# Optimization experiments

Hardware: AMD Instinct MI355X
Metric: run time of the kernel (lower is better)

The kernel has to match this reference:

```python
import jax, jax.numpy as jnp
import numpy as np

D = 1024      # model_dim
H = 16        # n_heads
BLOCK = 256   # block_dim
B, S = 4, 4096


def setup_inputs() -> dict:
    key = jax.random.key(0)
    ks = jax.random.split(key, 6)
    x = jax.random.normal(ks[0], (B, S, D), dtype=jnp.float32)
    # random permutation per batch row (mirrors torch.argsort(torch.rand(...)))
    rand_perm = jnp.argsort(jax.random.uniform(ks[1], (B, S)), axis=-1).astype(jnp.int32)
    W_in = jax.random.normal(ks[2], (D, 3 * D), dtype=jnp.float32) / np.float32(np.sqrt(D))
    b_in = jax.random.normal(ks[3], (3 * D,), dtype=jnp.float32) * 0.02
    W_out = jax.random.normal(ks[4], (D, D), dtype=jnp.float32) / np.float32(np.sqrt(D))
    b_out = jax.random.normal(ks[5], (D,), dtype=jnp.float32) * 0.02
    return {"x": x, "rand_perm": rand_perm, "W_in": W_in, "b_in": b_in,
            "W_out": W_out, "b_out": b_out}


def reference(x, rand_perm, W_in, b_in, W_out, b_out):
    Bb, Ss, Dm = x.shape
    dh = Dm // H
    nb = Ss // BLOCK  # S divisible by BLOCK -> no padding needed
    # permute sequence: x_rand[..., i, :] = x[..., perm[i], :]
    x_r = jnp.take_along_axis(x, rand_perm[..., None], axis=-2)          # [B,S,D]
    xb = x_r.reshape(Bb, nb, BLOCK, Dm)                                   # block-diagonal chunks
    qkv = jnp.einsum('bntd,de->bnte', xb, W_in) + b_in                    # [B,nb,blk,3D]
    # torch layout: chunk by head first, then (q,k,v) within head
    qkv = qkv.reshape(Bb, nb, BLOCK, H, 3, dh)
    q = jnp.moveaxis(qkv[..., 0, :], 3, 2)                                # [B,nb,H,blk,dh]
    k = jnp.moveaxis(qkv[..., 1, :], 3, 2)
    v = jnp.moveaxis(qkv[..., 2, :], 3, 2)
    scores = jnp.einsum('bnhtd,bnhsd->bnhts', q, k) / np.float32(np.sqrt(dh))
    att = jax.nn.softmax(scores, axis=-1)
    o = jnp.einsum('bnhts,bnhsd->bnhtd', att, v)                          # [B,nb,H,blk,dh]

    def merge(t):  # [B,nb,H,blk,dh] -> [B,S,D] (heads concatenated on feature dim)
        return jnp.moveaxis(t, 2, 3).reshape(Bb, Ss, Dm)

    o = merge(o) @ W_out + b_out
    k_f = merge(k)
    v_f = merge(v)
    # scatter back: out[perm[i]] = src[i]  <=>  out[j] = src[inv_perm[j]]
    inv = jnp.argsort(rand_perm, axis=-1)
    unperm = lambda t: jnp.take_along_axis(t, inv[..., None], axis=-2)
    return unperm(o), unperm(k_f), unperm(v_f)
```

## Files before the change

### kernel.cpp

```cpp
#include <hip/hip_runtime.h>

#define D_   1024
#define H_   16
#define DHd  64
#define BLK  256
#define B_   4
#define S_   4096
#define NB_  16
#define M_   16384
#define N1_  3072
#define NT_  32

typedef __attribute__((ext_vector_type(8))) short short8;
typedef __attribute__((ext_vector_type(4))) float f32x4;
typedef unsigned short u16;
typedef __attribute__((ext_vector_type(4))) unsigned short u16x4;

__device__ inline u16 f2bf(float f) {
  unsigned int u = __float_as_uint(f);
  unsigned int r = (u + 0x7fffu + ((u >> 16) & 1u)) >> 16;
  return (u16)r;
}

__device__ inline void async_ld16(const void* g, void* l) {
  __builtin_amdgcn_global_load_lds(
      (const __attribute__((address_space(1))) unsigned int*)g,
      (__attribute__((address_space(3))) unsigned int*)l, 16, 0, 0);
}

__global__ __launch_bounds__(256)
void permute_cast_kernel(const float* __restrict__ x, const int* __restrict__ perm,
                         u16* __restrict__ xp) {
  int bid = blockIdx.x;
  int b = bid >> 12;
  int i = bid & 4095;
  int prow = perm[b * S_ + i];
  const float4* src = reinterpret_cast<const float4*>(x + (size_t)(b * S_ + prow) * D_);
  float4 v = src[threadIdx.x];
  u16x4 o;
  o.x = f2bf(v.x); o.y = f2bf(v.y); o.z = f2bf(v.z); o.w = f2bf(v.w);
  reinterpret_cast<u16x4*>(xp + (size_t)bid * D_)[threadIdx.x] = o;
}

__global__ __launch_bounds__(256)
void transpose_cast_kernel(const float* __restrict__ src, u16* __restrict__ dst,
                           int R, int C) {
  __shared__ float tile[32][33];
  int tx = threadIdx.x, ty = threadIdx.y;
  int c0 = blockIdx.x * 32, r0 = blockIdx.y * 32;
  #pragma unroll
  for (int i = ty; i < 32; i += 8)
    tile[i][tx] = src[(size_t)(r0 + i) * C + c0 + tx];
  __syncthreads();
  #pragma unroll
  for (int i = ty; i < 32; i += 8)
    dst[(size_t)(c0 + i) * R + r0 + tx] = f2bf(tile[tx][i]);
}

template<int MODE>
__global__ __launch_bounds__(512, 2)
void gemm_kernel(const u16* __restrict__ A, const u16* __restrict__ BT,
                 const float* __restrict__ bias, const int* __restrict__ perm,
                 u16* __restrict__ q_ws, u16* __restrict__ k_ws, u16* __restrict__ vT_ws,
                 float* __restrict__ out_k, float* __restrict__ out_v,
                 float* __restrict__ out_o) {
  constexpr int NCOL = (MODE == 0) ? N1_ : D_;
  constexpr int NWG  = (M_ / 256) * (NCOL / 256);
  constexpr int CPX  = NWG / 8;

  __shared__ u16 LDS[4 * 16384];
  __shared__ int perm_l[256];

  const int tid  = threadIdx.x;
  const int lane = tid & 63;
  const int w    = tid >> 6;
  const int wr   = w >> 2, wc = w & 3;
  const int l4   = lane >> 4, l15 = lane & 15;

  const int orig = blockIdx.x;
  const int lid  = (orig & 7) * CPX + (orig >> 3);
  const int i0   = (lid & 63) * 256;
  const int n0   = (lid >> 6) * 256;
  const int bidx = i0 >> 12;

  if (tid < 256) perm_l[tid] = perm[bidx * S_ + (i0 & 4095) + tid];

  const int srow = tid >> 2;
  const int sq   = (tid & 3) ^ ((tid >> 3) & 3);
  const u16* pA0 = A  + (size_t)(i0 + srow) * 1024 + sq * 8;
  const u16* pA1 = pA0 + (size_t)128 * 1024;
  const u16* pB0 = BT + (size_t)(n0 + srow) * 1024 + sq * 8;
  const u16* pB1 = pB0 + (size_t)128 * 1024;

  const int ps   = l4 ^ ((l15 >> 1) & 3);
  const int aoff = (wr * 128 + l15) * 64 + ps * 16;
  const int boff = 16384 + (wc * 64 + l15) * 64 + ps * 16;

  f32x4 acc[8][4] = {};

  #define STAGE(kt, b) do {                                    \
    const int ko_ = (kt) * 32;                                 \
    u16* base_ = &LDS[(b) * 16384 + w * 512];                  \
    async_ld16(pA0 + ko_, base_);                              \
    async_ld16(pA1 + ko_, base_ + 4096);                       \
    async_ld16(pB0 + ko_, base_ + 8192);                       \
    async_ld16(pB1 + ko_, base_ + 12288);                      \
  } while (0)

  #define COMPUTE(b) do {                                                         \
    const char* lb_ = (const char*)LDS + (b) * 32768;                             \
    short8 af_[8], bf_[4];                                                        \
    _Pragma("unroll")                                                             \
    for (int m = 0; m < 8; ++m)                                                   \
      af_[m] = *reinterpret_cast<const short8*>(lb_ + aoff + m * 1024);           \
    bf_[0] = *reinterpret_cast<const short8*>(lb_ + boff);                        \
    bf_[1] = *reinterpret_cast<const short8*>(lb_ + boff + 1024);                 \
    __builtin_amdgcn_s_setprio(1);                                                \
    _Pragma("unroll")                                                             \
    for (int m = 0; m < 8; ++m) {                                                 \
      acc[m][0] = __builtin_amdgcn_mfma_f32_16x16x32_bf16(af_[m], bf_[0], acc[m][0], 0, 0, 0); \
      acc[m][1] = __builtin_amdgcn_mfma_f32_16x16x32_bf16(af_[m], bf_[1], acc[m][1], 0, 0, 0); \
    }                                                                             \
    __builtin_amdgcn_s_setprio(0);                                                \
    bf_[2] = *reinterpret_cast<const short8*>(lb_ + boff + 2048);                 \
    bf_[3] = *reinterpret_cast<const short8*>(lb_ + boff + 3072);                 \
    __builtin_amdgcn_s_setprio(1);                                                \
    _Pragma("unroll")                                                             \
    for (int m = 0; m < 8; ++m) {                                                 \
      acc[m][2] = __builtin_amdgcn_mfma_f32_16x16x32_bf16(af_[m], bf_[2], acc[m][2], 0, 0, 0); \
      acc[m][3] = __builtin_amdgcn_mfma_f32_16x16x32_bf16(af_[m], bf_[3], acc[m][3], 0, 0, 0); \
    }                                                                             \
    __builtin_amdgcn_s_setprio(0);                                                \
  } while (0)

  STAGE(0, 0);
  STAGE(1, 1);
  #pragma unroll 1
  for (int kt = 0; kt < NT_ - 2; ++kt) {
    STAGE(kt + 2, (kt + 2) & 3);
    asm volatile("s_waitcnt vmcnt(8) lgkmcnt(0)" ::: "memory");
    __builtin_amdgcn_s_barrier();
    COMPUTE(kt & 3);
  }
  asm volatile("s_waitcnt vmcnt(4) lgkmcnt(0)" ::: "memory");
  __builtin_amdgcn_s_barrier();
  COMPUTE((NT_ - 2) & 3);
  asm volatile("s_waitcnt vmcnt(0) lgkmcnt(0)" ::: "memory");
  __builtin_amdgcn_s_barrier();
  COMPUTE((NT_ - 1) & 3);
  #undef STAGE
  #undef COMPUTE

  if (MODE == 0) {
    #pragma unroll
    for (int n = 0; n < 4; ++n) {
      int col = n0 + wc * 64 + n * 16 + l15;
      float bias_v = bias[col];
      int h  = col / 192;
      int rem = col - h * 192;
      int cc = rem >> 6;
      int dd = rem & 63;
      int qcol = (h << 6) + dd;
      #pragma unroll
      for (int m = 0; m < 8; ++m) {
        int rbase = i0 + wr * 128 + m * 16 + l4 * 4;
        if (cc == 0) {
          #pragma unroll
          for (int r = 0; r < 4; ++r) {
            float val = acc[m][n][r] + bias_v;
            q_ws[(size_t)(rbase + r) * D_ + qcol] = f2bf(val);
          }
        } else if (cc == 1) {
          #pragma unroll
          for (int r = 0; r < 4; ++r) {
            float val = acc[m][n][r] + bias_v;
            int rr = rbase + r;
            k_ws[(size_t)rr * D_ + qcol] = f2bf(val);
            int prow = perm_l[rr - i0];
            out_k[(size_t)(bidx * S_ + prow) * D_ + qcol] = val;
          }
        } else {
          u16x4 pk;
          #pragma unroll
          for (int r = 0; r < 4; ++r) {
            float val = acc[m][n][r] + bias_v;
            int rr = rbase + r;
            int prow = perm_l[rr - i0];
            out_v[(size_t)(bidx * S_ + prow) * D_ + qcol] = val;
            pk[r] = f2bf(val);
          }
          int i_loc = rbase & 4095;
          int nblk = i_loc >> 8;
          int t    = i_loc & 255;
          *reinterpret_cast<u16x4*>(
              &vT_ws[((((size_t)bidx * NB_ + nblk) * H_ + h) * DHd + dd) * BLK + t]) = pk;
        }
      }
    }
  } else {
    #pragma unroll
    for (int n = 0; n < 4; ++n) {
      int col = n0 + wc * 64 + n * 16 + l15;
      float bias_v = bias[col];
      #pragma unroll
      for (int m = 0; m < 8; ++m) {
        int rbase = i0 + wr * 128 + m * 16 + l4 * 4;
        #pragma unroll
        for (int r = 0; r < 4; ++r) {
          int rr = rbase + r;
          int prow = perm_l[rr - i0];
          out_o[(size_t)(bidx * S_ + prow) * D_ + col] = acc[m][n][r] + bias_v;
        }
      }
    }
  }
}

__global__ __launch_bounds__(256)
void attn_kernel(const u16* __restrict__ q_ws, const u16* __restrict__ k_ws,
                 const u16* __restrict__ vT_ws, u16* __restrict__ o_ws) {
  __shared__ u16 P_lds[4 * 64 * 64];

  int bid  = blockIdx.x;
  int h    = bid & 15;
  int nblk = (bid >> 4) & 15;
  int b    = bid >> 8;
  int row0 = b * S_ + nblk * BLK;
  int lane = threadIdx.x & 63;
  int w    = threadIdx.x >> 6;
  int l4 = lane >> 4, l15 = lane & 15;

  const u16* qb  = q_ws + (size_t)row0 * D_ + h * 64;
  const u16* kb  = k_ws + (size_t)row0 * D_ + h * 64;
  const u16* vTb = vT_ws + ((size_t)(b * NB_ + nblk) * H_ + h) * (size_t)(DHd * BLK);

  short8 qf[4][2];
  #pragma unroll
  for (int mt = 0; mt < 4; ++mt)
    #pragma unroll
    for (int kk = 0; kk < 2; ++kk)
      qf[mt][kk] = *reinterpret_cast<const short8*>(
          qb + (size_t)(w * 64 + mt * 16 + l15) * D_ + kk * 32 + l4 * 8);

  f32x4 Oacc[4][4] = {};
  float mS[4][4], lS[4][4];
  #pragma unroll
  for (int mt = 0; mt < 4; ++mt)
    #pragma unroll
    for (int r = 0; r < 4; ++r) { mS[mt][r] = -1e30f; lS[mt][r] = 0.f; }

  for (int ct = 0; ct < 4; ++ct) {
    f32x4 Sc[4][4] = {};
    #pragma unroll
    for (int kk = 0; kk < 2; ++kk) {
      #pragma unroll
      for (int nt = 0; nt < 4; ++nt) {
        short8 kf = *reinterpret_cast<const short8*>(
            kb + (size_t)(ct * 64 + nt * 16 + l15) * D_ + kk * 32 + l4 * 8);
        #pragma unroll
        for (int mt = 0; mt < 4; ++mt)
          Sc[mt][nt] = __builtin_amdgcn_mfma_f32_16x16x32_bf16(qf[mt][kk], kf, Sc[mt][nt], 0, 0, 0);
      }
    }
    #pragma unroll
    for (int mt = 0; mt < 4; ++mt) {
      #pragma unroll
      for (int r = 0; r < 4; ++r) {
        float v0 = fmaxf(fmaxf(Sc[mt][0][r], Sc[mt][1][r]), fmaxf(Sc[mt][2][r], Sc[mt][3][r]));
        v0 *= 0.125f;
        v0 = fmaxf(v0, __shfl_xor(v0, 1));
        v0 = fmaxf(v0, __shfl_xor(v0, 2));
        v0 = fmaxf(v0, __shfl_xor(v0, 4));
        v0 = fmaxf(v0, __shfl_xor(v0, 8));
        float mn = fmaxf(mS[mt][r], v0);
        float alpha = __expf(mS[mt][r] - mn);
        mS[mt][r] = mn;
        float rs = 0.f;
        #pragma unroll
        for (int nt = 0; nt < 4; ++nt) {
          float p = __expf(Sc[mt][nt][r] * 0.125f - mn);
          Sc[mt][nt][r] = p;
          rs += p;
        }
        rs += __shfl_xor(rs, 1);
        rs += __shfl_xor(rs, 2);
        rs += __shfl_xor(rs, 4);
        rs += __shfl_xor(rs, 8);
        lS[mt][r] = lS[mt][r] * alpha + rs;
        #pragma unroll
        for (int nt = 0; nt < 4; ++nt)
          Oacc[mt][nt][r] *= alpha;
      }
    }
    #pragma unroll
    for (int mt = 0; mt < 4; ++mt)
      #pragma unroll
      for (int nt = 0; nt < 4; ++nt)
        #pragma unroll
        for (int r = 0; r < 4; ++r)
          P_lds[w * 4096 + (mt * 16 + l4 * 4 + r) * 64 + nt * 16 + l15] = f2bf(Sc[mt][nt][r]);
    #pragma unroll
    for (int kk = 0; kk < 2; ++kk) {
      short8 pa[4];
      #pragma unroll
      for (int mt = 0; mt < 4; ++mt)
        pa[mt] = *reinterpret_cast<const short8*>(
            &P_lds[w * 4096 + (mt * 16 + l15) * 64 + kk * 32 + l4 * 8]);
      #pragma unroll
      for (int nt = 0; nt < 4; ++nt) {
        short8 vf = *reinterpret_cast<const short8*>(
            vTb + (size_t)(nt * 16 + l15) * BLK + ct * 64 + kk * 32 + l4 * 8);
        #pragma unroll
        for (int mt = 0; mt < 4; ++mt)
          Oacc[mt][nt] = __builtin_amdgcn_mfma_f32_16x16x32_bf16(pa[mt], vf, Oacc[mt][nt], 0, 0, 0);
      }
    }
  }
  u16* ob = o_ws + (size_t)row0 * D_ + h * 64;
  #pragma unroll
  for (int mt = 0; mt < 4; ++mt)
    #pragma unroll
    for (int r = 0; r < 4; ++r) {
      float inv = 1.f / lS[mt][r];
      int row = w * 64 + mt * 16 + l4 * 4 + r;
      #pragma unroll
      for (int nt = 0; nt < 4; ++nt)
        ob[(size_t)row * D_ + nt * 16 + l15] = f2bf(Oacc[mt][nt][r] * inv);
    }
}

extern "C" void kernel_launch(void* const* d_in, const int* in_sizes, int n_in,
                              void* d_out, int out_size, void* d_ws, size_t ws_size,
                              hipStream_t stream) {
  const float* x     = (const float*)d_in[0];
  const int*   perm  = (const int*)d_in[1];
  const float* W_in  = (const float*)d_in[2];
  const float* b_in  = (const float*)d_in[3];
  const float* W_out = (const float*)d_in[4];
  const float* b_out = (const float*)d_in[5];

  float* out_o = (float*)d_out;
  float* out_k = out_o + (size_t)M_ * D_;
  float* out_v = out_k + (size_t)M_ * D_;

  const size_t nE = (size_t)M_ * D_;
  u16 *xp, *q_ws, *k_ws, *vT, *o_ws, *WinT, *WoutT;
  size_t need_full = (5 * nE + (size_t)N1_ * D_ + (size_t)D_ * D_) * 2;
  if (ws_size >= need_full) {
    u16* w = (u16*)d_ws;
    xp = w; q_ws = xp + nE; k_ws = q_ws + nE; vT = k_ws + nE; o_ws = vT + nE;
    WinT = o_ws + nE; WoutT = WinT + (size_t)N1_ * D_;
  } else {
    xp = (u16*)d_out; q_ws = xp + nE;
    u16* w = (u16*)d_ws;
    k_ws = w; vT = k_ws + nE; o_ws = vT + nE;
    WinT = o_ws + nE; WoutT = WinT + (size_t)N1_ * D_;
  }

  permute_cast_kernel<<<M_, 256, 0, stream>>>(x, perm, xp);
  transpose_cast_kernel<<<dim3(N1_ / 32, D_ / 32), dim3(32, 8), 0, stream>>>(W_in, WinT, D_, N1_);
  transpose_cast_kernel<<<dim3(D_ / 32, D_ / 32), dim3(32, 8), 0, stream>>>(W_out, WoutT, D_, D_);
  gemm_kernel<0><<<(M_ / 256) * (N1_ / 256), 512, 0, stream>>>(
      xp, WinT, b_in, perm, q_ws, k_ws, vT, out_k, out_v, nullptr);
  attn_kernel<<<B_ * NB_ * H_, 256, 0, stream>>>(q_ws, k_ws, vT, o_ws);
  gemm_kernel<1><<<(M_ / 256) * (D_ / 256), 512, 0, stream>>>(
      o_ws, WoutT, b_out, perm, nullptr, nullptr, nullptr, nullptr, nullptr, out_o);
}
```

Baseline: 322.8 us.

## Load A fragments directly from global into registers, stage only B in LDS

```diff
diff --git a/kernel.cpp b/kernel.cpp
--- a/kernel.cpp
+++ b/kernel.cpp
@@ -9,7 +9,7 @@
 #define NB_  16
 #define M_   16384
 #define N1_  3072
-#define NT_  32
+#define KT_  32
 
 typedef __attribute__((ext_vector_type(8))) short short8;
 typedef __attribute__((ext_vector_type(4))) float f32x4;
@@ -68,7 +68,7 @@
   constexpr int NWG  = (M_ / 256) * (NCOL / 256);
   constexpr int CPX  = NWG / 8;
 
-  __shared__ u16 LDS[4 * 16384];
+  __shared__ u16 LDS[4 * 8192];
   __shared__ int perm_l[256];
 
   const int tid  = threadIdx.x;
@@ -85,71 +85,73 @@
 
   if (tid < 256) perm_l[tid] = perm[bidx * S_ + (i0 & 4095) + tid];
 
-  const int srow = tid >> 2;
-  const int sq   = (tid & 3) ^ ((tid >> 3) & 3);
-  const u16* pA0 = A  + (size_t)(i0 + srow) * 1024 + sq * 8;
-  const u16* pA1 = pA0 + (size_t)128 * 1024;
-  const u16* pB0 = BT + (size_t)(n0 + srow) * 1024 + sq * 8;
-  const u16* pB1 = pB0 + (size_t)128 * 1024;
-
-  const int ps   = l4 ^ ((l15 >> 1) & 3);
-  const int aoff = (wr * 128 + l15) * 64 + ps * 16;
-  const int boff = 16384 + (wc * 64 + l15) * 64 + ps * 16;
+  const int sl = (((tid & 3) ^ ((tid >> 4) & 3)) << 3);
+  const u16* pB = BT + (size_t)(n0 + (tid >> 2)) * 1024 + sl;
+
+  const int pkq   = (l4 ^ (l15 >> 2)) * 16;
+  const int bbase = (wc * 64 + l15) * 64 + pkq;
+
+  const u16* pAw = A + (size_t)(i0 + wr * 128 + l15) * 1024 + l4 * 8;
 
   f32x4 acc[8][4] = {};
-
-  #define STAGE(kt, b) do {                                    \
-    const int ko_ = (kt) * 32;                                 \
-    u16* base_ = &LDS[(b) * 16384 + w * 512];                  \
-    async_ld16(pA0 + ko_, base_);                              \
-    async_ld16(pA1 + ko_, base_ + 4096);                       \
-    async_ld16(pB0 + ko_, base_ + 8192);                       \
-    async_ld16(pB1 + ko_, base_ + 12288);                      \
+  short8 afA[8], afB[8];
+
+  #define LOADA(dst, t) do {                                           \
+    _Pragma("unroll")                                                  \
+    for (int m = 0; m < 8; ++m)                                        \
+      dst[m] = *reinterpret_cast<const short8*>(pAw + (size_t)m * 16384 + (t) * 32); \
   } while (0)
 
-  #define COMPUTE(b) do {                                                         \
-    const char* lb_ = (const char*)LDS + (b) * 32768;                             \
-    short8 af_[8], bf_[4];                                                        \
-    _Pragma("unroll")                                                             \
-    for (int m = 0; m < 8; ++m)                                                   \
-      af_[m] = *reinterpret_cast<const short8*>(lb_ + aoff + m * 1024);           \
-    bf_[0] = *reinterpret_cast<const short8*>(lb_ + boff);                        \
-    bf_[1] = *reinterpret_cast<const short8*>(lb_ + boff + 1024);                 \
-    __builtin_amdgcn_s_setprio(1);                                                \
-    _Pragma("unroll")                                                             \
-    for (int m = 0; m < 8; ++m) {                                                 \
-      acc[m][0] = __builtin_amdgcn_mfma_f32_16x16x32_bf16(af_[m], bf_[0], acc[m][0], 0, 0, 0); \
-      acc[m][1] = __builtin_amdgcn_mfma_f32_16x16x32_bf16(af_[m], bf_[1], acc[m][1], 0, 0, 0); \
-    }                                                                             \
-    __builtin_amdgcn_s_setprio(0);                                                \
-    bf_[2] = *reinterpret_cast<const short8*>(lb_ + boff + 2048);                 \
-    bf_[3] = *reinterpret_cast<const short8*>(lb_ + boff + 3072);                 \
-    __builtin_amdgcn_s_setprio(1);                                                \
-    _Pragma("unroll")                                                             \
-    for (int m = 0; m < 8; ++m) {                                                 \
-      acc[m][2] = __builtin_amdgcn_mfma_f32_16x16x32_bf16(af_[m], bf_[2], acc[m][2], 0, 0, 0); \
-      acc[m][3] = __builtin_amdgcn_mfma_f32_16x16x32_bf16(af_[m], bf_[3], acc[m][3], 0, 0, 0); \
-    }                                                                             \
-    __builtin_amdgcn_s_setprio(0);                                                \
+  #define STAGE_B(t, b) do {                                           \
+    u16* d_ = &LDS[(b) * 8192 + w * 512];                              \
+    async_ld16(pB + (size_t)(t) * 32,              d_);                \
+    async_ld16(pB + (size_t)(t) * 32 + 128 * 1024, d_ + 4096);         \
   } while (0)
 
-  STAGE(0, 0);
-  STAGE(1, 1);
+  #define COMPUTE(t, af) do {                                          \
+    const char* lb_ = (const char*)LDS + ((t) & 3) * 16384;            \
+    short8 bf_[4];                                                     \
+    _Pragma("unroll")                                                  \
+    for (int n = 0; n < 4; ++n)                                        \
+      bf_[n] = *reinterpret_cast<const short8*>(lb_ + bbase + n * 1024); \
+    _Pragma("unroll")                                                  \
+    for (int n = 0; n < 4; ++n)                                        \
+      _Pragma("unroll")                                                \
+      for (int m = 0; m < 8; ++m)                                      \
+        acc[m][n] = __builtin_amdgcn_mfma_f32_16x16x32_bf16(af[m], bf_[n], acc[m][n], 0, 0, 0); \
+  } while (0)
+
+  #define VMW(n) asm volatile("s_waitcnt vmcnt(" #n ")" ::: "memory")
+
+  LOADA(afA, 0);
+  STAGE_B(0, 0); STAGE_B(1, 1); STAGE_B(2, 2);
+  VMW(4);
+  __builtin_amdgcn_s_barrier();
+
   #pragma unroll 1
-  for (int kt = 0; kt < NT_ - 2; ++kt) {
-    STAGE(kt + 2, (kt + 2) & 3);
-    asm volatile("s_waitcnt vmcnt(8) lgkmcnt(0)" ::: "memory");
-    __builtin_amdgcn_s_barrier();
-    COMPUTE(kt & 3);
+  for (int t = 0; t < KT_ - 4; t += 2) {
+    LOADA(afB, t + 1); STAGE_B(t + 3, (t + 3) & 3);
+    COMPUTE(t, afA);
+    VMW(2); __builtin_amdgcn_s_barrier();
+    LOADA(afA, t + 2); STAGE_B(t + 4, (t + 4) & 3);
+    COMPUTE(t + 1, afB);
+    VMW(2); __builtin_amdgcn_s_barrier();
   }
-  asm volatile("s_waitcnt vmcnt(4) lgkmcnt(0)" ::: "memory");
-  __builtin_amdgcn_s_barrier();
-  COMPUTE((NT_ - 2) & 3);
-  asm volatile("s_waitcnt vmcnt(0) lgkmcnt(0)" ::: "memory");
-  __builtin_amdgcn_s_barrier();
-  COMPUTE((NT_ - 1) & 3);
-  #undef STAGE
+  LOADA(afB, 29); STAGE_B(31, 3);
+  COMPUTE(28, afA);
+  VMW(2); __builtin_amdgcn_s_barrier();
+  LOADA(afA, 30);
+  COMPUTE(29, afB);
+  VMW(2); __builtin_amdgcn_s_barrier();
+  LOADA(afB, 31);
+  COMPUTE(30, afA);
+  VMW(0); __builtin_amdgcn_s_barrier();
+  COMPUTE(31, afB);
+
+  #undef LOADA
+  #undef STAGE_B
   #undef COMPUTE
+  #undef VMW
 
   if (MODE == 0) {
     #pragma unroll
@@ -166,10 +168,8 @@
         int rbase = i0 + wr * 128 + m * 16 + l4 * 4;
         if (cc == 0) {
           #pragma unroll
-          for (int r = 0; r < 4; ++r) {
-            float val = acc[m][n][r] + bias_v;
-            q_ws[(size_t)(rbase + r) * D_ + qcol] = f2bf(val);
-          }
+          for (int r = 0; r < 4; ++r)
+            q_ws[(size_t)(rbase + r) * D_ + qcol] = f2bf(acc[m][n][r] + bias_v);
         } else if (cc == 1) {
           #pragma unroll
           for (int r = 0; r < 4; ++r) {
```

After: 478.4 us. +48.2%, slower.
